# Kernel tuning notes

Measured on AMD Instinct MI355X. Metric: run time of the kernel, lower is better.

Reference implementation:

```python
import jax, jax.numpy as jnp
import numpy as np

NUM_HEADS = 16
HEAD_DIM = 64
BSZ, SEQ, EMBED = 2, 2048, NUM_HEADS * HEAD_DIM
SCALE = HEAD_DIM ** (-0.5)
NEG = -1e9  # large negative for masked positions (finite, fp16-unsafe values avoided)


def setup_inputs() -> dict:
    key = jax.random.key(0)
    kq, kk, kv = jax.random.split(key, 3)
    q = jax.random.normal(kq, (BSZ, SEQ, EMBED), dtype=jnp.float32)
    k = jax.random.normal(kk, (BSZ, SEQ, EMBED), dtype=jnp.float32)
    v = jax.random.normal(kv, (BSZ, SEQ, EMBED), dtype=jnp.float32)
    # additive causal mask: 0 on/below diagonal, NEG above, shape (bsz,1,tgt,src)
    causal = jnp.where(jnp.tril(jnp.ones((SEQ, SEQ), dtype=bool)), 0.0, NEG).astype(jnp.float32)
    causal = jnp.broadcast_to(causal[None, None], (BSZ, 1, SEQ, SEQ))
    return {"query_states": q, "key_states": k, "value_states": v,
            "causal_attention_mask": causal}


def reference(query_states, key_states, value_states, causal_attention_mask):
    bsz, tgt_len, embed_dim = query_states.shape
    # [b, h, s, d]
    def shape_heads(t):
        return t.reshape(bsz, -1, NUM_HEADS, HEAD_DIM).transpose(0, 2, 1, 3)
    q = shape_heads(query_states * SCALE)
    k = shape_heads(key_states)
    v = shape_heads(value_states)
    # scores: [b, h, tgt, src]
    attn_weights = jnp.einsum('bhqd,bhkd->bhqk', q, k)
    attn_weights = attn_weights + causal_attention_mask  # broadcast over heads
    attn_probs = jax.nn.softmax(attn_weights, axis=-1)
    # dropout p=0.0 / eval mode -> identity
    attn_output = jnp.einsum('bhqk,bhkd->bhqd', attn_probs, v)
    attn_output = attn_output.transpose(0, 2, 1, 3).reshape(bsz, tgt_len, embed_dim)
    return attn_output
```

## Files before the change

kernel.cpp:

```cpp
#include <hip/hip_runtime.h>
#include <hip/hip_bf16.h>
#include <stdint.h>

#define BSZ 2
#define SEQ 2048
#define NHEADS 16
#define HDIM 64
#define EMBED (NHEADS * HDIM)
#define NQT 32

#define QSCALE 0.1803368801111244f
#define C2 11.5416914f

typedef unsigned short u16;
typedef unsigned int u32;
typedef __attribute__((ext_vector_type(8))) short bf16x8;
typedef __attribute__((ext_vector_type(16))) float f32x16;

#define TILE_B 8192
#define WSV_OFF (8ull * 1024 * 1024)

__device__ __forceinline__ u32 pkbf(float x, float y) {
  union { __hip_bfloat162 h; u32 u; } c;
  c.h = __float22bfloat162_rn(make_float2(x, y));
  return c.u;
}

__device__ __forceinline__ void gload16(const void* g, void* l) {
  __builtin_amdgcn_global_load_lds(
      (const __attribute__((address_space(1))) u32*)g,
      (__attribute__((address_space(3))) u32*)l, 16, 0, 0);
}

__global__ __launch_bounds__(256) void prep_kv(const float* __restrict__ K,
                                               const float* __restrict__ V,
                                               char* __restrict__ ws) {
  __shared__ float tile[64][68];
  if (blockIdx.x < 2048) {
    const int t = blockIdx.x * 256 + threadIdx.x;
    const int c = t & 7;
    const int h = (t >> 3) & 15;
    const size_t bs = (size_t)(t >> 7);
    const int s = (int)(bs & 2047);
    const int b = (int)(bs >> 11);
    const float* p = K + bs * EMBED + h * HDIM + c * 8;
    const float4 a = *reinterpret_cast<const float4*>(p);
    const float4 d = *reinterpret_cast<const float4*>(p + 4);
    uint4 out;
    out.x = pkbf(a.x, a.y); out.y = pkbf(a.z, a.w);
    out.z = pkbf(d.x, d.y); out.w = pkbf(d.z, d.w);
    const int kt = s >> 6, key = s & 63;
    const int kb = key >> 5;
    const int ks = c >> 1, hi = c & 1;
    const int lane = hi * 32 + (key & 31);
    char* dst = ws + ((size_t)(b * 16 + h) * 32 + kt) * TILE_B +
                ((kb * 4 + ks) * 64 + lane) * 16;
    *reinterpret_cast<uint4*>(dst) = out;
  } else {
    const int blk = blockIdx.x - 2048;
    const int kt = blk & 31, bh = blk >> 5;
    const int b = bh >> 4, h = bh & 15;
    const float* src = V + ((size_t)b * SEQ + kt * 64) * EMBED + h * HDIM;
    const int t = threadIdx.x;
    {
      const int row = t >> 2, c0 = (t & 3) * 16;
      const float* p = src + (size_t)row * EMBED + c0;
#pragma unroll
      for (int j = 0; j < 4; ++j)
        *reinterpret_cast<float4*>(&tile[row][c0 + 4 * j]) =
            *reinterpret_cast<const float4*>(p + 4 * j);
    }
    __syncthreads();
    const int d = t & 63;
#pragma unroll
    for (int halfc = 0; halfc < 2; ++halfc) {
      const int kc = (t >> 6) + halfc * 4;
      const int kb = kc >> 2, hi = kc & 1;
      const int ka0 = kc * 8;
      const int base = kb * 32 + (ka0 & 16) + hi * 4;
      uint4 out;
      out.x = pkbf(tile[base + 0][d], tile[base + 1][d]);
      out.y = pkbf(tile[base + 2][d], tile[base + 3][d]);
      out.z = pkbf(tile[base + 8][d], tile[base + 9][d]);
      out.w = pkbf(tile[base + 10][d], tile[base + 11][d]);
      const int lane = hi * 32 + (d & 31);
      const int db = d >> 5;
      const int ks2 = (kc >> 1) & 1;
      char* dst = ws + WSV_OFF + ((size_t)bh * 32 + kt) * TILE_B +
                  ((kb * 4 + ks2 * 2 + db) * 64 + lane) * 16;
      *reinterpret_cast<uint4*>(dst) = out;
    }
  }
}

__device__ __forceinline__ void stream_step(const char* Kc, const char* Vc,
                                            const bf16x8 q0, const bf16x8 q1,
                                            const bf16x8 q2, const bf16x8 q3,
                                            f32x16& o0, f32x16& o1, float& lsum,
                                            int kb, int l, int lq, int hi,
                                            bool diagq) {
  f32x16 s = {};
  __builtin_amdgcn_s_setprio(1);
  {
    const bf16x8 kf0 = *reinterpret_cast<const bf16x8*>(Kc + ((kb * 4 + 0) * 64 + l) * 16);
    s = __builtin_amdgcn_mfma_f32_32x32x16_bf16(kf0, q0, s, 0, 0, 0);
    const bf16x8 kf1 = *reinterpret_cast<const bf16x8*>(Kc + ((kb * 4 + 1) * 64 + l) * 16);
    s = __builtin_amdgcn_mfma_f32_32x32x16_bf16(kf1, q1, s, 0, 0, 0);
    const bf16x8 kf2 = *reinterpret_cast<const bf16x8*>(Kc + ((kb * 4 + 2) * 64 + l) * 16);
    s = __builtin_amdgcn_mfma_f32_32x32x16_bf16(kf2, q2, s, 0, 0, 0);
    const bf16x8 kf3 = *reinterpret_cast<const bf16x8*>(Kc + ((kb * 4 + 3) * 64 + l) * 16);
    s = __builtin_amdgcn_mfma_f32_32x32x16_bf16(kf3, q3, s, 0, 0, 0);
  }
  __builtin_amdgcn_s_setprio(0);

  if (diagq) {
#pragma unroll
    for (int r = 0; r < 16; ++r) {
      const int crow = (r & 3) + 8 * (r >> 2) + 4 * hi;
      if (crow > lq) s[r] = -1.0e30f;
    }
  }

  float e[16];
#pragma unroll
  for (int r = 0; r < 16; ++r) e[r] = __builtin_amdgcn_exp2f(s[r] - C2);
  lsum += ((e[0] + e[1]) + (e[2] + e[3])) + ((e[4] + e[5]) + (e[6] + e[7])) +
          ((e[8] + e[9]) + (e[10] + e[11])) + ((e[12] + e[13]) + (e[14] + e[15]));
  union { u32 w[4]; bf16x8 v; } pa0, pa1;
#pragma unroll
  for (int i = 0; i < 4; ++i) {
    pa0.w[i] = pkbf(e[2 * i], e[2 * i + 1]);
    pa1.w[i] = pkbf(e[8 + 2 * i], e[8 + 2 * i + 1]);
  }

  __builtin_amdgcn_s_setprio(1);
  {
    const bf16x8 v00 = *reinterpret_cast<const bf16x8*>(Vc + ((kb * 4 + 0) * 64 + l) * 16);
    o0 = __builtin_amdgcn_mfma_f32_32x32x16_bf16(pa0.v, v00, o0, 0, 0, 0);
    const bf16x8 v01 = *reinterpret_cast<const bf16x8*>(Vc + ((kb * 4 + 1) * 64 + l) * 16);
    o1 = __builtin_amdgcn_mfma_f32_32x32x16_bf16(pa0.v, v01, o1, 0, 0, 0);
    const bf16x8 v10 = *reinterpret_cast<const bf16x8*>(Vc + ((kb * 4 + 2) * 64 + l) * 16);
    o0 = __builtin_amdgcn_mfma_f32_32x32x16_bf16(pa1.v, v10, o0, 0, 0, 0);
    const bf16x8 v11 = *reinterpret_cast<const bf16x8*>(Vc + ((kb * 4 + 3) * 64 + l) * 16);
    o1 = __builtin_amdgcn_mfma_f32_32x32x16_bf16(pa1.v, v11, o1, 0, 0, 0);
  }
  __builtin_amdgcn_s_setprio(0);
}

__device__ __forceinline__ void write_stream(float* __restrict__ O, int b, int h,
                                             int qt, int qhalf, int lq, int hi,
                                             int l, const f32x16& o0,
                                             const f32x16& o1,
                                             const float* __restrict__ Obuf,
                                             float linv) {
  float* outg = O + ((size_t)b * SEQ + qt * 64 + qhalf * 32) * EMBED + h * HDIM;
#pragma unroll
  for (int r = 0; r < 16; ++r) {
    const int crow = (r & 3) + 8 * (r >> 2) + 4 * hi;
    const float il = __shfl(linv, crow, 64);
    const float v0 = (o0[r] + Obuf[r * 64 + l]) * il;
    const float v1 = (o1[r] + Obuf[1024 + r * 64 + l]) * il;
    outg[(size_t)crow * EMBED + lq] = v0;
    outg[(size_t)crow * EMBED + 32 + lq] = v1;
  }
}

__global__ __launch_bounds__(256, 2) void mha_fwd(const float* __restrict__ Q,
                                                  const char* __restrict__ ws,
                                                  float* __restrict__ O) {
  __shared__ __align__(16) char smem[33280];

  const int id = ((blockIdx.x & 7) << 6) | (blockIdx.x >> 3);
  const int qlo = id & 15, bh = id >> 4;
  const int qhi = (NQT - 1) - qlo;
  const int b = bh >> 4, h = bh & 15;

  const int wv = threadIdx.x >> 6;
  const int l = threadIdx.x & 63;
  const int qhalf = wv & 1, kb = wv >> 1;
  const int lq = l & 31;
  const int hi = l >> 5;

  bf16x8 qh[4], ql[4];
  {
    union { uint4 u; bf16x8 v; } cv;
#pragma unroll
    for (int st = 0; st < 2; ++st) {
      const int qt = st ? qlo : qhi;
      const float* qp =
          Q + ((size_t)b * SEQ + qt * 64 + qhalf * 32 + lq) * EMBED + h * HDIM + hi * 8;
#pragma unroll
      for (int ks = 0; ks < 4; ++ks) {
        const float4 a = *reinterpret_cast<const float4*>(qp + ks * 16);
        const float4 d = *reinterpret_cast<const float4*>(qp + ks * 16 + 4);
        cv.u.x = pkbf(a.x * QSCALE, a.y * QSCALE);
        cv.u.y = pkbf(a.z * QSCALE, a.w * QSCALE);
        cv.u.z = pkbf(d.x * QSCALE, d.y * QSCALE);
        cv.u.w = pkbf(d.z * QSCALE, d.w * QSCALE);
        if (st) ql[ks] = cv.v; else qh[ks] = cv.v;
      }
    }
  }

  const char* gK = ws + (size_t)bh * 32 * TILE_B;
  const char* gV = ws + WSV_OFF + (size_t)bh * 32 * TILE_B;

#define STAGE(dstoff, src)                                                    \
  {                                                                           \
    const char* s_ = (src);                                                   \
    gload16(s_ + wv * 2048 + l * 16, smem + (dstoff) + wv * 2048);            \
    gload16(s_ + wv * 2048 + 1024 + l * 16, smem + (dstoff) + wv * 2048 + 1024); \
  }

  STAGE(0, gK);
  STAGE(16384, gV);
  __syncthreads();

  f32x16 oh0 = {}, oh1 = {}, ol0 = {}, ol1 = {};
  float lsh = 0.f, lsl = 0.f;

  int cur = 0;
  for (int kt = 0; kt <= qhi; ++kt) {
    const bool more = kt < qhi;
    if (more) {
      STAGE((cur ^ 1) * 8192, gK + (size_t)(kt + 1) * TILE_B);
      STAGE(16384 + (cur ^ 1) * 8192, gV + (size_t)(kt + 1) * TILE_B);
    }
    const char* Kc = smem + cur * 8192;
    const char* Vc = smem + 16384 + cur * 8192;

    {
      const bool diag = (kt == qhi);
      if (!(diag && kb == 1 && qhalf == 0))
        stream_step(Kc, Vc, qh[0], qh[1], qh[2], qh[3], oh0, oh1, lsh,
                    kb, l, lq, hi, diag && (kb == qhalf));
    }
    if (kt <= qlo) {
      const bool diag = (kt == qlo);
      if (!(diag && kb == 1 && qhalf == 0))
        stream_step(Kc, Vc, ql[0], ql[1], ql[2], ql[3], ol0, ol1, lsl,
                    kb, l, lq, hi, diag && (kb == qhalf));
    }

    if (more) __syncthreads();
    cur ^= 1;
  }

  __syncthreads();
  const float l2h = lsh + __shfl_xor(lsh, 32, 64);
  const float l2l = lsl + __shfl_xor(lsl, 32, 64);
  float* Obuf = reinterpret_cast<float*>(smem);
  float* Lbuf = reinterpret_cast<float*>(smem + 32768);

  if (kb == 1) {
#pragma unroll
    for (int r = 0; r < 16; ++r) {
      Obuf[(qhalf * 2 + 0) * 1024 + r * 64 + l] = oh0[r];
      Obuf[(qhalf * 2 + 1) * 1024 + r * 64 + l] = oh1[r];
      Obuf[((2 + qhalf) * 2 + 0) * 1024 + r * 64 + l] = ol0[r];
      Obuf[((2 + qhalf) * 2 + 1) * 1024 + r * 64 + l] = ol1[r];
    }
    if (l < 32) {
      Lbuf[qhalf * 32 + lq] = l2h;
      Lbuf[(2 + qhalf) * 32 + lq] = l2l;
    }
  }
  __syncthreads();
  if (kb == 0) {
    const float linv_h = 1.0f / (l2h + Lbuf[qhalf * 32 + lq]);
    write_stream(O, b, h, qhi, qhalf, lq, hi, l, oh0, oh1,
                 Obuf + (qhalf * 2) * 1024, linv_h);
    const float linv_l = 1.0f / (l2l + Lbuf[(2 + qhalf) * 32 + lq]);
    write_stream(O, b, h, qlo, qhalf, lq, hi, l, ol0, ol1,
                 Obuf + ((2 + qhalf) * 2) * 1024, linv_l);
  }
#undef STAGE
}

extern "C" void kernel_launch(void* const* d_in, const int* in_sizes, int n_in,
                              void* d_out, int out_size, void* d_ws, size_t ws_size,
                              hipStream_t stream) {
  const float* q = (const float*)d_in[0];
  const float* k = (const float*)d_in[1];
  const float* v = (const float*)d_in[2];
  float* o = (float*)d_out;
  char* ws = (char*)d_ws;

  prep_kv<<<dim3(3072), dim3(256), 0, stream>>>(k, v, ws);
  mha_fwd<<<dim3(512), dim3(256), 0, stream>>>(q, ws, o);
}
```

Baseline: 50.59 us.

## Stage two KV tiles per barrier and interleave hi/lo query streams

Shared memory grows to four K/V slots so two tiles are staged per iteration and the block synchronizes once per pair of tiles instead of once per tile. A new dual step issues the QK^T and PV MFMAs for both query tiles (high and low) back to back, sharing each K/V fragment load between them and interleaving independent MFMA chains. The goal is fewer barriers, fewer LDS reads and more instruction-level parallelism. The cost is doubled LDS use (about 66KB per block), which may limit two blocks per CU, plus higher register pressure.

New measurement: 53.25 us. 5.3% more time.

```diff
diff --git a/kernel.cpp b/kernel.cpp
--- a/kernel.cpp
+++ b/kernel.cpp
@@ -93,34 +93,26 @@
   }
 }
 
-__device__ __forceinline__ void stream_step(const char* Kc, const char* Vc,
-                                            const bf16x8 q0, const bf16x8 q1,
-                                            const bf16x8 q2, const bf16x8 q3,
-                                            f32x16& o0, f32x16& o1, float& lsum,
-                                            int kb, int l, int lq, int hi,
-                                            bool diagq) {
+__device__ __forceinline__ void step_one(const char* Kc, const char* Vc,
+                                         const bf16x8* q,
+                                         f32x16& o0, f32x16& o1, float& lsum,
+                                         int kb, int l, int hi, bool mask) {
   f32x16 s = {};
   __builtin_amdgcn_s_setprio(1);
-  {
-    const bf16x8 kf0 = *reinterpret_cast<const bf16x8*>(Kc + ((kb * 4 + 0) * 64 + l) * 16);
-    s = __builtin_amdgcn_mfma_f32_32x32x16_bf16(kf0, q0, s, 0, 0, 0);
-    const bf16x8 kf1 = *reinterpret_cast<const bf16x8*>(Kc + ((kb * 4 + 1) * 64 + l) * 16);
-    s = __builtin_amdgcn_mfma_f32_32x32x16_bf16(kf1, q1, s, 0, 0, 0);
-    const bf16x8 kf2 = *reinterpret_cast<const bf16x8*>(Kc + ((kb * 4 + 2) * 64 + l) * 16);
-    s = __builtin_amdgcn_mfma_f32_32x32x16_bf16(kf2, q2, s, 0, 0, 0);
-    const bf16x8 kf3 = *reinterpret_cast<const bf16x8*>(Kc + ((kb * 4 + 3) * 64 + l) * 16);
-    s = __builtin_amdgcn_mfma_f32_32x32x16_bf16(kf3, q3, s, 0, 0, 0);
+#pragma unroll
+  for (int i = 0; i < 4; ++i) {
+    const bf16x8 kf = *reinterpret_cast<const bf16x8*>(Kc + ((kb * 4 + i) * 64 + l) * 16);
+    s = __builtin_amdgcn_mfma_f32_32x32x16_bf16(kf, q[i], s, 0, 0, 0);
   }
   __builtin_amdgcn_s_setprio(0);
-
-  if (diagq) {
+  if (mask) {
+    const int lq = l & 31;
 #pragma unroll
     for (int r = 0; r < 16; ++r) {
       const int crow = (r & 3) + 8 * (r >> 2) + 4 * hi;
       if (crow > lq) s[r] = -1.0e30f;
     }
   }
-
   float e[16];
 #pragma unroll
   for (int r = 0; r < 16; ++r) e[r] = __builtin_amdgcn_exp2f(s[r] - C2);
@@ -132,17 +124,80 @@
     pa0.w[i] = pkbf(e[2 * i], e[2 * i + 1]);
     pa1.w[i] = pkbf(e[8 + 2 * i], e[8 + 2 * i + 1]);
   }
-
   __builtin_amdgcn_s_setprio(1);
+#pragma unroll
+  for (int i = 0; i < 4; ++i) {
+    const bf16x8 vf = *reinterpret_cast<const bf16x8*>(Vc + ((kb * 4 + i) * 64 + l) * 16);
+    f32x16& o = (i & 1) ? o1 : o0;
+    o = __builtin_amdgcn_mfma_f32_32x32x16_bf16((i >> 1) ? pa1.v : pa0.v, vf, o, 0, 0, 0);
+  }
+  __builtin_amdgcn_s_setprio(0);
+}
+
+__device__ __forceinline__ void step_dual(const char* Kc, const char* Vc,
+                                          const bf16x8* qh, const bf16x8* ql,
+                                          f32x16& oh0, f32x16& oh1,
+                                          f32x16& ol0, f32x16& ol1,
+                                          float& lsh, float& lsl,
+                                          int kb, int l, int hi,
+                                          bool mask_h, bool mask_l) {
+  f32x16 sh = {}, sl = {};
+  __builtin_amdgcn_s_setprio(1);
+#pragma unroll
+  for (int i = 0; i < 4; ++i) {
+    const bf16x8 kf = *reinterpret_cast<const bf16x8*>(Kc + ((kb * 4 + i) * 64 + l) * 16);
+    sh = __builtin_amdgcn_mfma_f32_32x32x16_bf16(kf, qh[i], sh, 0, 0, 0);
+    sl = __builtin_amdgcn_mfma_f32_32x32x16_bf16(kf, ql[i], sl, 0, 0, 0);
+  }
+  __builtin_amdgcn_s_setprio(0);
+  const int lq = l & 31;
+  if (mask_h) {
+#pragma unroll
+    for (int r = 0; r < 16; ++r) {
+      const int crow = (r & 3) + 8 * (r >> 2) + 4 * hi;
+      if (crow > lq) sh[r] = -1.0e30f;
+    }
+  }
+  if (mask_l) {
+#pragma unroll
+    for (int r = 0; r < 16; ++r) {
+      const int crow = (r & 3) + 8 * (r >> 2) + 4 * hi;
+      if (crow > lq) sl[r] = -1.0e30f;
+    }
+  }
+  union { u32 w[4]; bf16x8 v; } ph0, ph1, pl0, pl1;
   {
-    const bf16x8 v00 = *reinterpret_cast<const bf16x8*>(Vc + ((kb * 4 + 0) * 64 + l) * 16);
-    o0 = __builtin_amdgcn_mfma_f32_32x32x16_bf16(pa0.v, v00, o0, 0, 0, 0);
-    const bf16x8 v01 = *reinterpret_cast<const bf16x8*>(Vc + ((kb * 4 + 1) * 64 + l) * 16);
-    o1 = __builtin_amdgcn_mfma_f32_32x32x16_bf16(pa0.v, v01, o1, 0, 0, 0);
-    const bf16x8 v10 = *reinterpret_cast<const bf16x8*>(Vc + ((kb * 4 + 2) * 64 + l) * 16);
-    o0 = __builtin_amdgcn_mfma_f32_32x32x16_bf16(pa1.v, v10, o0, 0, 0, 0);
-    const bf16x8 v11 = *reinterpret_cast<const bf16x8*>(Vc + ((kb * 4 + 3) * 64 + l) * 16);
-    o1 = __builtin_amdgcn_mfma_f32_32x32x16_bf16(pa1.v, v11, o1, 0, 0, 0);
+    float e[16];
+#pragma unroll
+    for (int r = 0; r < 16; ++r) e[r] = __builtin_amdgcn_exp2f(sh[r] - C2);
+    lsh += ((e[0] + e[1]) + (e[2] + e[3])) + ((e[4] + e[5]) + (e[6] + e[7])) +
+           ((e[8] + e[9]) + (e[10] + e[11])) + ((e[12] + e[13]) + (e[14] + e[15]));
+#pragma unroll
+    for (int i = 0; i < 4; ++i) {
+      ph0.w[i] = pkbf(e[2 * i], e[2 * i + 1]);
+      ph1.w[i] = pkbf(e[8 + 2 * i], e[8 + 2 * i + 1]);
+    }
+  }
+  {
+    float e[16];
+#pragma unroll
+    for (int r = 0; r < 16; ++r) e[r] = __builtin_amdgcn_exp2f(sl[r] - C2);
+    lsl += ((e[0] + e[1]) + (e[2] + e[3])) + ((e[4] + e[5]) + (e[6] + e[7])) +
+           ((e[8] + e[9]) + (e[10] + e[11])) + ((e[12] + e[13]) + (e[14] + e[15]));
+#pragma unroll
+    for (int i = 0; i < 4; ++i) {
+      pl0.w[i] = pkbf(e[2 * i], e[2 * i + 1]);
+      pl1.w[i] = pkbf(e[8 + 2 * i], e[8 + 2 * i + 1]);
+    }
+  }
+  __builtin_amdgcn_s_setprio(1);
+#pragma unroll
+  for (int i = 0; i < 4; ++i) {
+    const bf16x8 vf = *reinterpret_cast<const bf16x8*>(Vc + ((kb * 4 + i) * 64 + l) * 16);
+    f32x16& oh = (i & 1) ? oh1 : oh0;
+    f32x16& ol = (i & 1) ? ol1 : ol0;
+    oh = __builtin_amdgcn_mfma_f32_32x32x16_bf16((i >> 1) ? ph1.v : ph0.v, vf, oh, 0, 0, 0);
+    ol = __builtin_amdgcn_mfma_f32_32x32x16_bf16((i >> 1) ? pl1.v : pl0.v, vf, ol, 0, 0, 0);
   }
   __builtin_amdgcn_s_setprio(0);
 }
@@ -168,7 +223,7 @@
 __global__ __launch_bounds__(256, 2) void mha_fwd(const float* __restrict__ Q,
                                                   const char* __restrict__ ws,
                                                   float* __restrict__ O) {
-  __shared__ __align__(16) char smem[33280];
+  __shared__ __align__(16) char smem[66048];
 
   const int id = ((blockIdx.x & 7) << 6) | (blockIdx.x >> 3);
   const int qlo = id & 15, bh = id >> 4;
@@ -205,52 +260,54 @@
   const char* gK = ws + (size_t)bh * 32 * TILE_B;
   const char* gV = ws + WSV_OFF + (size_t)bh * 32 * TILE_B;
 
-#define STAGE(dstoff, src)                                                    \
-  {                                                                           \
-    const char* s_ = (src);                                                   \
-    gload16(s_ + wv * 2048 + l * 16, smem + (dstoff) + wv * 2048);            \
-    gload16(s_ + wv * 2048 + 1024 + l * 16, smem + (dstoff) + wv * 2048 + 1024); \
-  }
-
-  STAGE(0, gK);
-  STAGE(16384, gV);
-  __syncthreads();
+#define STAGE(slot, t_)                                                        \
+  {                                                                            \
+    const char* sK = gK + (size_t)(t_) * TILE_B;                               \
+    const char* sV = gV + (size_t)(t_) * TILE_B;                               \
+    char* dK = smem + (slot) * 8192 + wv * 2048;                               \
+    char* dV = smem + 32768 + (slot) * 8192 + wv * 2048;                       \
+    gload16(sK + wv * 2048 + l * 16, dK);                                      \
+    gload16(sK + wv * 2048 + 1024 + l * 16, dK + 1024);                        \
+    gload16(sV + wv * 2048 + l * 16, dV);                                      \
+    gload16(sV + wv * 2048 + 1024 + l * 16, dV + 1024);                        \
+  }
 
   f32x16 oh0 = {}, oh1 = {}, ol0 = {}, ol1 = {};
   float lsh = 0.f, lsl = 0.f;
 
-  int cur = 0;
-  for (int kt = 0; kt <= qhi; ++kt) {
-    const bool more = kt < qhi;
-    if (more) {
-      STAGE((cur ^ 1) * 8192, gK + (size_t)(kt + 1) * TILE_B);
-      STAGE(16384 + (cur ^ 1) * 8192, gV + (size_t)(kt + 1) * TILE_B);
-    }
-    const char* Kc = smem + cur * 8192;
-    const char* Vc = smem + 16384 + cur * 8192;
-
-    {
-      const bool diag = (kt == qhi);
-      if (!(diag && kb == 1 && qhalf == 0))
-        stream_step(Kc, Vc, qh[0], qh[1], qh[2], qh[3], oh0, oh1, lsh,
-                    kb, l, lq, hi, diag && (kb == qhalf));
-    }
-    if (kt <= qlo) {
-      const bool diag = (kt == qlo);
-      if (!(diag && kb == 1 && qhalf == 0))
-        stream_step(Kc, Vc, ql[0], ql[1], ql[2], ql[3], ol0, ol1, lsl,
-                    kb, l, lq, hi, diag && (kb == qhalf));
-    }
-
-    if (more) __syncthreads();
-    cur ^= 1;
-  }
-
+#define PROCESS(t_)                                                            \
+  {                                                                            \
+    const int t = (t_);                                                        \
+    const char* Kc = smem + (t & 3) * 8192;                                    \
+    const char* Vc = smem + 32768 + (t & 3) * 8192;                            \
+    const bool dh = (t == qhi), dl = (t == qlo);                               \
+    const bool live_h = !(dh && kb == 1 && qhalf == 0);                        \
+    const bool live_l = (t <= qlo) && !(dl && kb == 1 && qhalf == 0);          \
+    if (live_h && live_l)                                                      \
+      step_dual(Kc, Vc, qh, ql, oh0, oh1, ol0, ol1, lsh, lsl, kb, l, hi,       \
+                dh && (kb == qhalf), dl && (kb == qhalf));                     \
+    else if (live_h)                                                           \
+      step_one(Kc, Vc, qh, oh0, oh1, lsh, kb, l, hi, dh && (kb == qhalf));     \
+    else if (live_l)                                                           \
+      step_one(Kc, Vc, ql, ol0, ol1, lsl, kb, l, hi, dl && (kb == qhalf));     \
+  }
+
+  STAGE(0, 0);
+  STAGE(1, 1);
   __syncthreads();
+
+  for (int kt = 0; kt <= qhi; kt += 2) {
+    if (kt + 2 <= qhi) STAGE((kt + 2) & 3, kt + 2);
+    if (kt + 3 <= qhi) STAGE((kt + 3) & 3, kt + 3);
+    PROCESS(kt);
+    if (kt + 1 <= qhi) PROCESS(kt + 1);
+    __syncthreads();
+  }
+
   const float l2h = lsh + __shfl_xor(lsh, 32, 64);
   const float l2l = lsl + __shfl_xor(lsl, 32, 64);
   float* Obuf = reinterpret_cast<float*>(smem);
-  float* Lbuf = reinterpret_cast<float*>(smem + 32768);
+  float* Lbuf = reinterpret_cast<float*>(smem + 65536);
 
   if (kb == 1) {
 #pragma unroll
@@ -275,6 +332,7 @@
                  Obuf + ((2 + qhalf) * 2) * 1024, linv_l);
   }
 #undef STAGE
+#undef PROCESS
 }
 
 extern "C" void kernel_launch(void* const* d_in, const int* in_sizes, int n_in,
```

## Split KV loop into two parity partitions with separate combine kernel

Applied to the files above, without the earlier changes.

Each attention block now handles only even or odd key tiles, doubling the grid to 1024 blocks. The partial outputs are stored as bf16 in workspace along with row sums, and a new combine kernel adds the two halves, normalises, and writes fp32 output. The aim is more parallelism and better occupancy, since launch bounds now allow 4 blocks per CU. The cost is an extra launch, the workspace round trip, and bf16 rounding of the unnormalised partial sums.

New measurement: 59.35 us. 1.17x slower.

```diff
diff --git a/kernel.cpp b/kernel.cpp
--- a/kernel.cpp
+++ b/kernel.cpp
@@ -19,11 +19,21 @@
 
 #define TILE_B 8192
 #define WSV_OFF (8ull * 1024 * 1024)
+#define WSO_OFF (16ull * 1024 * 1024)
+#define WSO_PAR_U16 (4ull * 1024 * 1024)
+#define WSL_OFF (32ull * 1024 * 1024)
 
 __device__ __forceinline__ u32 pkbf(float x, float y) {
   union { __hip_bfloat162 h; u32 u; } c;
   c.h = __float22bfloat162_rn(make_float2(x, y));
   return c.u;
+}
+
+__device__ __forceinline__ u16 f2bf(float x) {
+  union { float f; u32 u; } v;
+  v.f = x;
+  u32 r = v.u + 0x7fffu + ((v.u >> 16) & 1u);
+  return (u16)(r >> 16);
 }
 
 __device__ __forceinline__ void gload16(const void* g, void* l) {
@@ -147,31 +157,14 @@
   __builtin_amdgcn_s_setprio(0);
 }
 
-__device__ __forceinline__ void write_stream(float* __restrict__ O, int b, int h,
-                                             int qt, int qhalf, int lq, int hi,
-                                             int l, const f32x16& o0,
-                                             const f32x16& o1,
-                                             const float* __restrict__ Obuf,
-                                             float linv) {
-  float* outg = O + ((size_t)b * SEQ + qt * 64 + qhalf * 32) * EMBED + h * HDIM;
-#pragma unroll
-  for (int r = 0; r < 16; ++r) {
-    const int crow = (r & 3) + 8 * (r >> 2) + 4 * hi;
-    const float il = __shfl(linv, crow, 64);
-    const float v0 = (o0[r] + Obuf[r * 64 + l]) * il;
-    const float v1 = (o1[r] + Obuf[1024 + r * 64 + l]) * il;
-    outg[(size_t)crow * EMBED + lq] = v0;
-    outg[(size_t)crow * EMBED + 32 + lq] = v1;
-  }
-}
-
-__global__ __launch_bounds__(256, 2) void mha_fwd(const float* __restrict__ Q,
-                                                  const char* __restrict__ ws,
-                                                  float* __restrict__ O) {
+__global__ __launch_bounds__(256, 4) void mha_fwd(const float* __restrict__ Q,
+                                                  char* __restrict__ ws) {
   __shared__ __align__(16) char smem[33280];
 
-  const int id = ((blockIdx.x & 7) << 6) | (blockIdx.x >> 3);
-  const int qlo = id & 15, bh = id >> 4;
+  const int id = ((blockIdx.x & 7) << 7) | (blockIdx.x >> 3);
+  const int par = id & 1;
+  const int qlo = (id >> 1) & 15;
+  const int bh = id >> 5;
   const int qhi = (NQT - 1) - qlo;
   const int b = bh >> 4, h = bh & 15;
 
@@ -205,27 +198,28 @@
   const char* gK = ws + (size_t)bh * 32 * TILE_B;
   const char* gV = ws + WSV_OFF + (size_t)bh * 32 * TILE_B;
 
-#define STAGE(dstoff, src)                                                    \
-  {                                                                           \
-    const char* s_ = (src);                                                   \
-    gload16(s_ + wv * 2048 + l * 16, smem + (dstoff) + wv * 2048);            \
-    gload16(s_ + wv * 2048 + 1024 + l * 16, smem + (dstoff) + wv * 2048 + 1024); \
-  }
-
-  STAGE(0, gK);
-  STAGE(16384, gV);
+#define STAGE(slot, t_)                                                        \
+  {                                                                            \
+    const char* sK = gK + (size_t)(t_) * TILE_B;                               \
+    const char* sV = gV + (size_t)(t_) * TILE_B;                               \
+    char* dK = smem + (slot) * 8192 + wv * 2048;                               \
+    char* dV = smem + 16384 + (slot) * 8192 + wv * 2048;                       \
+    gload16(sK + wv * 2048 + l * 16, dK);                                      \
+    gload16(sK + wv * 2048 + 1024 + l * 16, dK + 1024);                        \
+    gload16(sV + wv * 2048 + l * 16, dV);                                      \
+    gload16(sV + wv * 2048 + 1024 + l * 16, dV + 1024);                        \
+  }
+
+  STAGE(0, par);
   __syncthreads();
 
   f32x16 oh0 = {}, oh1 = {}, ol0 = {}, ol1 = {};
   float lsh = 0.f, lsl = 0.f;
 
   int cur = 0;
-  for (int kt = 0; kt <= qhi; ++kt) {
-    const bool more = kt < qhi;
-    if (more) {
-      STAGE((cur ^ 1) * 8192, gK + (size_t)(kt + 1) * TILE_B);
-      STAGE(16384 + (cur ^ 1) * 8192, gV + (size_t)(kt + 1) * TILE_B);
-    }
+  for (int kt = par; kt <= qhi; kt += 2) {
+    const bool more = (kt + 2 <= qhi);
+    if (more) STAGE(cur ^ 1, kt + 2);
     const char* Kc = smem + cur * 8192;
     const char* Vc = smem + 16384 + cur * 8192;
 
@@ -267,14 +261,49 @@
   }
   __syncthreads();
   if (kb == 0) {
-    const float linv_h = 1.0f / (l2h + Lbuf[qhalf * 32 + lq]);
-    write_stream(O, b, h, qhi, qhalf, lq, hi, l, oh0, oh1,
-                 Obuf + (qhalf * 2) * 1024, linv_h);
-    const float linv_l = 1.0f / (l2l + Lbuf[(2 + qhalf) * 32 + lq]);
-    write_stream(O, b, h, qlo, qhalf, lq, hi, l, ol0, ol1,
-                 Obuf + ((2 + qhalf) * 2) * 1024, linv_l);
+    u16* wsO = reinterpret_cast<u16*>(ws + WSO_OFF) + (size_t)par * WSO_PAR_U16;
+    float* wsL = reinterpret_cast<float*>(ws + WSL_OFF) + (size_t)par * 65536;
+#pragma unroll
+    for (int st = 0; st < 2; ++st) {
+      const int qt = st ? qlo : qhi;
+      const f32x16& o0 = st ? ol0 : oh0;
+      const f32x16& o1 = st ? ol1 : oh1;
+      const float* Ob = Obuf + ((st ? 2 + qhalf : qhalf) * 2) * 1024;
+      const float lfull = (st ? l2l : l2h) + Lbuf[(st ? 2 + qhalf : qhalf) * 32 + lq];
+      const size_t base = ((size_t)bh * 32 + qt) * 64 + qhalf * 32;
+#pragma unroll
+      for (int r = 0; r < 16; ++r) {
+        const int crow = (r & 3) + 8 * (r >> 2) + 4 * hi;
+        wsO[(base + crow) * 64 + lq] = f2bf(o0[r] + Ob[r * 64 + l]);
+        wsO[(base + crow) * 64 + 32 + lq] = f2bf(o1[r] + Ob[1024 + r * 64 + l]);
+      }
+      if (hi == 0) wsL[base + lq] = lfull;
+    }
   }
 #undef STAGE
+}
+
+__global__ __launch_bounds__(256) void mha_combine(const char* __restrict__ ws,
+                                                   float* __restrict__ O) {
+  const int R0 = blockIdx.x * 8 + (threadIdx.x >> 5);
+  const int dp = (threadIdx.x & 31) * 2;
+  const u16* wsO = reinterpret_cast<const u16*>(ws + WSO_OFF);
+  const float* wsL = reinterpret_cast<const float*>(ws + WSL_OFF);
+  const u32 a = *reinterpret_cast<const u32*>(wsO + (size_t)R0 * 64 + dp);
+  const u32 bb = *reinterpret_cast<const u32*>(wsO + WSO_PAR_U16 +
+                                               (size_t)R0 * 64 + dp);
+  const float inv = 1.0f / (wsL[R0] + wsL[65536 + R0]);
+  union { u32 u; float f; } c0, c1, d0, d1;
+  c0.u = (a & 0xffffu) << 16;  c1.u = a & 0xffff0000u;
+  d0.u = (bb & 0xffffu) << 16; d1.u = bb & 0xffff0000u;
+  const float o0 = (c0.f + d0.f) * inv;
+  const float o1 = (c1.f + d1.f) * inv;
+  const int bh = R0 >> 11, qt = (R0 >> 6) & 31, row = R0 & 63;
+  const int q = qt * 64 + row;
+  const int b = bh >> 4, h = bh & 15;
+  float* out = O + ((size_t)b * SEQ + q) * EMBED + h * HDIM + dp;
+  out[0] = o0;
+  out[1] = o1;
 }
 
 extern "C" void kernel_launch(void* const* d_in, const int* in_sizes, int n_in,
@@ -287,5 +316,6 @@
   char* ws = (char*)d_ws;
 
   prep_kv<<<dim3(3072), dim3(256), 0, stream>>>(k, v, ws);
-  mha_fwd<<<dim3(512), dim3(256), 0, stream>>>(q, ws, o);
-}
+  mha_fwd<<<dim3(1024), dim3(256), 0, stream>>>(q, ws);
+  mha_combine<<<dim3(8192), dim3(256), 0, stream>>>(ws, o);
+}
```

## Deepen K/V LDS pipeline to four slots with prefetch distance two

Applied to the files above, without the earlier changes.

Replaces the double-buffered K/V staging with a four-slot ring in LDS, issuing loads two tiles ahead and using explicit vmcnt waits plus raw s_barrier instead of __syncthreads. This is meant to hide more global-to-LDS latency behind the MFMA work of each step. LDS use doubles to about 66KB per block, which may limit the two-blocks-per-CU occupancy, and the hand-counted vmcnt values must match the loads actually issued.

Result: slower. 55.74 us (+10.2%).

```diff
diff --git a/kernel.cpp b/kernel.cpp
--- a/kernel.cpp
+++ b/kernel.cpp
@@ -168,7 +168,7 @@
 __global__ __launch_bounds__(256, 2) void mha_fwd(const float* __restrict__ Q,
                                                   const char* __restrict__ ws,
                                                   float* __restrict__ O) {
-  __shared__ __align__(16) char smem[33280];
+  __shared__ __align__(16) char smem[66048];
 
   const int id = ((blockIdx.x & 7) << 6) | (blockIdx.x >> 3);
   const int qlo = id & 15, bh = id >> 4;
@@ -205,52 +205,60 @@
   const char* gK = ws + (size_t)bh * 32 * TILE_B;
   const char* gV = ws + WSV_OFF + (size_t)bh * 32 * TILE_B;
 
-#define STAGE(dstoff, src)                                                    \
-  {                                                                           \
-    const char* s_ = (src);                                                   \
-    gload16(s_ + wv * 2048 + l * 16, smem + (dstoff) + wv * 2048);            \
-    gload16(s_ + wv * 2048 + 1024 + l * 16, smem + (dstoff) + wv * 2048 + 1024); \
-  }
-
-  STAGE(0, gK);
-  STAGE(16384, gV);
-  __syncthreads();
+#define STAGE(slot, t_)                                                        \
+  {                                                                            \
+    const char* sK = gK + (size_t)(t_) * TILE_B;                               \
+    const char* sV = gV + (size_t)(t_) * TILE_B;                               \
+    char* dK = smem + (slot) * 8192 + wv * 2048;                               \
+    char* dV = smem + 32768 + (slot) * 8192 + wv * 2048;                       \
+    gload16(sK + wv * 2048 + l * 16, dK);                                      \
+    gload16(sK + wv * 2048 + 1024 + l * 16, dK + 1024);                        \
+    gload16(sV + wv * 2048 + l * 16, dV);                                      \
+    gload16(sV + wv * 2048 + 1024 + l * 16, dV + 1024);                        \
+  }
 
   f32x16 oh0 = {}, oh1 = {}, ol0 = {}, ol1 = {};
   float lsh = 0.f, lsl = 0.f;
 
-  int cur = 0;
+#define PROCESS(t_)                                                            \
+  {                                                                            \
+    const int t = (t_);                                                        \
+    const char* Kc = smem + (t & 3) * 8192;                                    \
+    const char* Vc = smem + 32768 + (t & 3) * 8192;                            \
+    const bool dh = (t == qhi), dl = (t == qlo);                               \
+    const bool live_l = (t <= qlo) && !(dl && kb == 1 && qhalf == 0);          \
+    if (!(dh && kb == 1 && qhalf == 0))                                        \
+      stream_step(Kc, Vc, qh[0], qh[1], qh[2], qh[3], oh0, oh1, lsh,           \
+                  kb, l, lq, hi, dh && (kb == qhalf));                         \
+    if (live_l)                                                                \
+      stream_step(Kc, Vc, ql[0], ql[1], ql[2], ql[3], ol0, ol1, lsl,           \
+                  kb, l, lq, hi, dl && (kb == qhalf));                         \
+  }
+
+  STAGE(0, 0);
+  STAGE(1, 1);
+  asm volatile("s_waitcnt vmcnt(8)" ::: "memory");
+  __builtin_amdgcn_s_barrier();
+  __builtin_amdgcn_sched_barrier(0);
+
   for (int kt = 0; kt <= qhi; ++kt) {
-    const bool more = kt < qhi;
-    if (more) {
-      STAGE((cur ^ 1) * 8192, gK + (size_t)(kt + 1) * TILE_B);
-      STAGE(16384 + (cur ^ 1) * 8192, gV + (size_t)(kt + 1) * TILE_B);
-    }
-    const char* Kc = smem + cur * 8192;
-    const char* Vc = smem + 16384 + cur * 8192;
-
-    {
-      const bool diag = (kt == qhi);
-      if (!(diag && kb == 1 && qhalf == 0))
-        stream_step(Kc, Vc, qh[0], qh[1], qh[2], qh[3], oh0, oh1, lsh,
-                    kb, l, lq, hi, diag && (kb == qhalf));
-    }
-    if (kt <= qlo) {
-      const bool diag = (kt == qlo);
-      if (!(diag && kb == 1 && qhalf == 0))
-        stream_step(Kc, Vc, ql[0], ql[1], ql[2], ql[3], ol0, ol1, lsl,
-                    kb, l, lq, hi, diag && (kb == qhalf));
-    }
-
-    if (more) __syncthreads();
-    cur ^= 1;
+    if (kt + 2 <= qhi) {
+      STAGE((kt + 2) & 3, kt + 2);
+      PROCESS(kt);
+      asm volatile("s_waitcnt vmcnt(8)" ::: "memory");
+    } else {
+      PROCESS(kt);
+      asm volatile("s_waitcnt vmcnt(0)" ::: "memory");
+    }
+    __builtin_amdgcn_s_barrier();
+    __builtin_amdgcn_sched_barrier(0);
   }
 
   __syncthreads();
   const float l2h = lsh + __shfl_xor(lsh, 32, 64);
   const float l2l = lsl + __shfl_xor(lsl, 32, 64);
   float* Obuf = reinterpret_cast<float*>(smem);
-  float* Lbuf = reinterpret_cast<float*>(smem + 32768);
+  float* Lbuf = reinterpret_cast<float*>(smem + 65536);
 
   if (kb == 1) {
 #pragma unroll
@@ -275,6 +283,7 @@
                  Obuf + ((2 + qhalf) * 2) * 1024, linv_l);
   }
 #undef STAGE
+#undef PROCESS
 }
 
 extern "C" void kernel_launch(void* const* d_in, const int* in_sizes, int n_in,
```
